# Kernel optimization log

Measured on AMD Instinct MI355X. Metric: run time of the kernel, lower is better.

Reference implementation:

```python
import jax, jax.numpy as jnp
import numpy as np

NUM_HEADS = 8
EPS = 1e-6


def setup_inputs() -> dict:
    key0 = jax.random.key(0)
    ks = jax.random.split(key0, 12)
    B, E, Hs, Ws, L = 8, 512, 32, 32, 1024
    s = 0.02
    return {
        "query": jax.random.normal(ks[0], (B, E, Hs, Ws), dtype=jnp.float32),
        "key": jax.random.normal(ks[1], (B, L, E), dtype=jnp.float32),
        "value": jax.random.normal(ks[2], (B, L, E), dtype=jnp.float32),
        # 1x1 conv for Q (kernel_size=1) stored as (E_out, E_in)
        "Wq": jax.random.normal(ks[3], (E, E), dtype=jnp.float32) * s,
        "bq": jnp.zeros((E,), dtype=jnp.float32),
        "Wk": jax.random.normal(ks[4], (E, E), dtype=jnp.float32) * s,
        "bk": jnp.zeros((E,), dtype=jnp.float32),
        "Wv": jax.random.normal(ks[5], (E, E), dtype=jnp.float32) * s,
        "bv": jnp.zeros((E,), dtype=jnp.float32),
        # out_conv: 1x1 conv + RMSNorm gain
        "Wo": jax.random.normal(ks[6], (E, E), dtype=jnp.float32) * s,
        "bo": jnp.zeros((E,), dtype=jnp.float32),
        "g": jnp.ones((E,), dtype=jnp.float32),
    }


def reference(query, key, value, Wq, bq, Wk, bk, Wv, bv, Wo, bo, g):
    B, E, Hs, Ws = query.shape
    H = NUM_HEADS
    Dh = E // H
    N = Hs * Ws
    # Q: 1x1 conv == per-pixel linear over channels
    Q = jnp.einsum('oi,bihw->bohw', Wq, query) + bq[None, :, None, None]
    # K, V: linear on last dim
    K = key @ Wk.T + bk      # (B, L, E)
    V = value @ Wv.T + bv    # (B, L, E)
    # faithful to torch .view: row-major reshape then transpose(2,3)
    Qh = Q.reshape(B, H, Dh, N).transpose(0, 1, 3, 2)        # (B, H, N, Dh)
    Kh = K.reshape(B, H, Dh, -1).transpose(0, 1, 3, 2)       # (B, H, L, Dh)
    Vh = V.reshape(B, H, Dh, -1).transpose(0, 1, 3, 2)       # (B, H, L, Dh)
    scores = jnp.einsum('bhnd,bhmd->bhnm', Qh, Kh) / jnp.sqrt(jnp.float32(Dh))
    attn = jax.nn.softmax(scores, axis=-1)
    out = jnp.einsum('bhnm,bhmd->bhnd', attn, Vh)            # (B, H, N, Dh)
    out = out.transpose(0, 1, 3, 2).reshape(B, E, Hs, Ws)
    # out_conv: 1x1 conv then channel-wise RMSNorm
    out = jnp.einsum('oi,bihw->bohw', Wo, out) + bo[None, :, None, None]
    rms = jnp.sqrt(jnp.mean(out * out, axis=1, keepdims=True) + EPS)
    return out / rms * g[None, :, None, None]
```

## Files before the change

kernel.cpp:

```cpp
#include <hip/hip_runtime.h>
#include <hip/hip_bf16.h>

namespace {

constexpr int kB  = 8;
constexpr int kE  = 512;
constexpr int kH  = 8;
constexpr int kDh = 64;
constexpr int kN  = 1024;
constexpr int kL  = 1024;

typedef __attribute__((ext_vector_type(8))) short short8;
typedef __attribute__((ext_vector_type(4))) float f32x4;
typedef __attribute__((ext_vector_type(4))) unsigned short ushort4v;

__device__ __forceinline__ unsigned short f2bf(float f) {
  unsigned u = __builtin_bit_cast(unsigned, f);
  u = (u + 0x7fffu + ((u >> 16) & 1u)) >> 16;
  return (unsigned short)u;
}

__device__ __forceinline__ f32x4 mfma16(short8 a, short8 b, f32x4 c) {
  return __builtin_amdgcn_mfma_f32_16x16x32_bf16(a, b, c, 0, 0, 0);
}

__device__ __forceinline__ void gl_lds16(const unsigned short* g, unsigned short* l) {
  __builtin_amdgcn_global_load_lds(
      (const __attribute__((address_space(1))) unsigned int*)g,
      (__attribute__((address_space(3))) unsigned int*)l, 16, 0, 0);
}

__global__ __launch_bounds__(256)
void convert_w(const float* __restrict__ w0, const float* __restrict__ w1,
               const float* __restrict__ w2, const float* __restrict__ w3,
               unsigned short* __restrict__ dst)
{
  const float* s = (blockIdx.y == 0) ? w0 : (blockIdx.y == 1) ? w1
                  : (blockIdx.y == 2) ? w2 : w3;
  unsigned short* d = dst + (size_t)blockIdx.y * 262144;
  const size_t i = ((size_t)blockIdx.x * 256 + threadIdx.x) * 4;
  const float4 v = *(const float4*)(s + i);
  ushort4v o = { f2bf(v.x), f2bf(v.y), f2bf(v.z), f2bf(v.w) };
  *(ushort4v*)(d + i) = o;
}

__global__ __launch_bounds__(256)
void convert_kv(const float* __restrict__ k, const float* __restrict__ v,
                unsigned short* __restrict__ dst)
{
  const float* s = blockIdx.y ? v : k;
  unsigned short* d = dst + (size_t)blockIdx.y * 4194304;
  const int flat = blockIdx.x * 256 + threadIdx.x;
  #pragma unroll
  for (int it = 0; it < 4; ++it) {
    const size_t i = ((size_t)flat + (size_t)it * 262144) * 4;
    const float4 x = *(const float4*)(s + i);
    ushort4v o = { f2bf(x.x), f2bf(x.y), f2bf(x.z), f2bf(x.w) };
    *(ushort4v*)(d + i) = o;
  }
}

__global__ __launch_bounds__(256)
void convert_qT(const float* __restrict__ q, unsigned short* __restrict__ qT)
{
  const int b = blockIdx.z, e0 = blockIdx.y * 32, n0 = blockIdx.x * 32;
  __shared__ float T[32][33];
  const int r  = threadIdx.x >> 3;
  const int c4 = (threadIdx.x & 7) * 4;
  const float4 v = *(const float4*)&q[((size_t)b * kE + e0 + r) * kN + n0 + c4];
  T[r][c4+0] = v.x; T[r][c4+1] = v.y; T[r][c4+2] = v.z; T[r][c4+3] = v.w;
  __syncthreads();
  ushort4v o = { f2bf(T[c4+0][r]), f2bf(T[c4+1][r]),
                 f2bf(T[c4+2][r]), f2bf(T[c4+3][r]) };
  *(ushort4v*)&qT[((size_t)b * kN + n0 + r) * kE + e0 + c4] = o;
}

__global__ __launch_bounds__(256)
void qkv_proj(const unsigned short* __restrict__ Wb4,
              const float* __restrict__ bq, const float* __restrict__ bk,
              const float* __restrict__ bv,
              const unsigned short* __restrict__ qT,
              const unsigned short* __restrict__ keyB,
              const unsigned short* __restrict__ valB,
              unsigned short* __restrict__ Qh,
              unsigned short* __restrict__ Kh,
              unsigned short* __restrict__ Vt)
{
  const int b    = blockIdx.z;
  const int mode = blockIdx.y >> 2;
  const int o0   = (blockIdx.y & 3) * 128;
  const int c0   = blockIdx.x * 128;
  const int wid  = threadIdx.x >> 6;
  const int lane = threadIdx.x & 63;
  const int lr = lane & 15, lg = lane >> 4;
  const int rbase = (wid >> 1) * 64;
  const int cbase = (wid & 1) * 64;

  __shared__ unsigned short smem[18432];

  const unsigned short* Wb   = Wb4 + (size_t)mode * 262144;
  const float*          bias = (mode == 0) ? bq : (mode == 1) ? bk : bv;
  const unsigned short* X    = (mode == 0) ? qT : (mode == 1) ? keyB : valB;

  const unsigned short* Wg = Wb + (size_t)o0 * kE;
  const unsigned short* Xg = X + ((size_t)b * 1024 + c0) * kE;

  const int srow = lane >> 2;
  const int sch  = lane & 3;

  auto stage = [&](int buf, int k0) {
    #pragma unroll
    for (int c = 0; c < 2; ++c) {
      const int row = wid * 32 + c * 16 + srow;
      const int koff = k0 + (((sch) ^ (row & 3)) << 3);
      gl_lds16(Wg + (size_t)row * kE + koff,
               &smem[buf * 8192 + (wid * 32 + c * 16) * 32]);
      gl_lds16(Xg + (size_t)row * kE + koff,
               &smem[buf * 8192 + 4096 + (wid * 32 + c * 16) * 32]);
    }
  };

  const f32x4 z = {0.f, 0.f, 0.f, 0.f};
  f32x4 acc[4][4];
  #pragma unroll
  for (int i = 0; i < 4; ++i)
    #pragma unroll
    for (int j = 0; j < 4; ++j) acc[i][j] = z;

  stage(0, 0);
  __syncthreads();

  for (int kt = 0; kt < 16; ++kt) {
    const int buf = kt & 1;
    if (kt < 15) stage(buf ^ 1, (kt + 1) * 32);

    short8 a[4], bfr[4];
    #pragma unroll
    for (int fr = 0; fr < 4; ++fr) {
      const int row = rbase + fr * 16 + lr;
      a[fr] = *(const short8*)&smem[buf * 8192 + row * 32 + ((lg ^ (row & 3)) << 3)];
    }
    #pragma unroll
    for (int fc = 0; fc < 4; ++fc) {
      const int row = cbase + fc * 16 + lr;
      bfr[fc] = *(const short8*)&smem[buf * 8192 + 4096 + row * 32 + ((lg ^ (row & 3)) << 3)];
    }
    #pragma unroll
    for (int fr = 0; fr < 4; ++fr)
      #pragma unroll
      for (int fc = 0; fc < 4; ++fc)
        acc[fr][fc] = mfma16(a[fr], bfr[fc], acc[fr][fc]);

    __syncthreads();
  }

  unsigned short* Ts = smem;
  #pragma unroll
  for (int fr = 0; fr < 4; ++fr) {
    #pragma unroll
    for (int j = 0; j < 4; ++j) {
      const int ol = rbase + fr * 16 + 4 * lg + j;
      const int o  = o0 + ol;
      const float bvv = bias[o];
      #pragma unroll
      for (int fc = 0; fc < 4; ++fc) {
        const int cl = cbase + fc * 16 + lr;
        float val = acc[fr][fc][j] + bvv;
        int addr;
        if (mode == 0) {
          const int hl = ol >> 6, d = o & 63;
          const int r = hl * 128 + cl;
          addr = r * 72 + ((((d >> 3) ^ (r & 7)) << 3) | (d & 7));
          val *= 0.125f;
        } else if (mode == 1) {
          const int seg = cl & 1, d = cl >> 1;
          const int r = seg * 128 + ol;
          addr = r * 72 + ((((d >> 3) ^ (r & 7)) << 3) | (d & 7));
        } else {
          const int r = cl;
          addr = r * 136 + ((((ol >> 3) ^ (r & 15)) << 3) | (ol & 7));
        }
        Ts[addr] = f2bf(val);
      }
    }
  }
  __syncthreads();

  const int hseg = c0 >> 7;
  #pragma unroll
  for (int it = 0; it < 8; ++it) {
    const int q = it * 256 + threadIdx.x;
    if (mode != 2) {
      const int r = q >> 3, ch = q & 7;
      const short8 vv = *(const short8*)&Ts[r * 72 + ((ch ^ (r & 7)) << 3)];
      if (mode == 0) {
        const int hl = r >> 7, n = r & 127;
        *(short8*)&Qh[((size_t)(b * kH + (o0 >> 6) + hl) * kN + c0 + n) * kDh + ch * 8] = vv;
      } else {
        const int seg = r >> 7, ml = r & 127;
        *(short8*)&Kh[((size_t)(b * kH + hseg) * kL + seg * 512 + o0 + ml) * kDh + ch * 8] = vv;
      }
    } else {
      const int r = q >> 4, ch = q & 15;
      const short8 vv = *(const short8*)&Ts[r * 136 + ((ch ^ (r & 15)) << 3)];
      const int d = r >> 1, half = r & 1;
      *(short8*)&Vt[((size_t)(b * kH + hseg) * kDh + d) * kL + half * 512 + o0 + ch * 8] = vv;
    }
  }
}

__global__ __launch_bounds__(256)
void attn_mfma(const unsigned short* __restrict__ Qh,
               const unsigned short* __restrict__ Kh,
               const unsigned short* __restrict__ Vt,
               unsigned short* __restrict__ AO)
{
  const int bh = blockIdx.x;
  const int h = bh & 7, b = bh >> 3;
  const int n0 = blockIdx.y * 128;
  const int tid  = threadIdx.x;
  const int wid  = tid >> 6;
  const int lane = tid & 63;
  const int lr = lane & 15, lg = lane >> 4;

  __shared__ unsigned short Ks[2][64 * 64];
  __shared__ unsigned short Vs[2][64 * 64];
  __shared__ unsigned short Pst[4][2][16 * 72];

  const unsigned short* Qp = Qh + ((size_t)(b * kH + h) * kN + n0 + wid * 32) * kDh;
  const unsigned short* Kp = Kh + (size_t)(b * kH + h) * kL * kDh;
  const unsigned short* Vp = Vt + (size_t)(b * kH + h) * kDh * kL;

  short8 aq[2][2];
  #pragma unroll
  for (int rf = 0; rf < 2; ++rf) {
    aq[rf][0] = *(const short8*)(Qp + (size_t)(rf * 16 + lr) * kDh + lg * 8);
    aq[rf][1] = *(const short8*)(Qp + (size_t)(rf * 16 + lr) * kDh + 32 + lg * 8);
  }

  const int srow8 = lane >> 3;
  const int sc16  = lane & 7;

  auto stageK = [&](int buf, int m0) {
    #pragma unroll
    for (int c = 0; c < 2; ++c) {
      const int row = wid * 16 + c * 8 + srow8;
      const unsigned short* src =
          Kp + (size_t)(m0 + row) * kDh + ((sc16 ^ (row & 7)) << 3);
      gl_lds16(src, &Ks[buf][(wid * 16 + c * 8) * 64]);
    }
  };
  auto stageV = [&](int buf, int m0) {
    #pragma unroll
    for (int c = 0; c < 2; ++c) {
      const int row = wid * 16 + c * 8 + srow8;
      const unsigned short* src =
          Vp + (size_t)row * kL + m0 + ((sc16 ^ (row & 7)) << 3);
      gl_lds16(src, &Vs[buf][(wid * 16 + c * 8) * 64]);
    }
  };

  const f32x4 z = {0.f, 0.f, 0.f, 0.f};
  f32x4 oacc[2][4];
  #pragma unroll
  for (int rf = 0; rf < 2; ++rf)
    #pragma unroll
    for (int dt = 0; dt < 4; ++dt) oacc[rf][dt] = z;
  f32x4 psum[2] = {z, z};

  stageK(0, 0);
  stageV(0, 0);
  __syncthreads();

  for (int kt = 0; kt < 16; ++kt) {
    const int cur = kt & 1;
    if (kt < 15) {
      stageK(cur ^ 1, (kt + 1) * 64);
      stageV(cur ^ 1, (kt + 1) * 64);
    }

    #pragma unroll
    for (int rf = 0; rf < 2; ++rf) {
      f32x4 s[4] = {z, z, z, z};
      #pragma unroll
      for (int t = 0; t < 4; ++t) {
        const int row = t * 16 + lr;
        const short8 bk0 = *(const short8*)&Ks[cur][row * 64 + (((lg    ) ^ (row & 7)) << 3)];
        const short8 bk1 = *(const short8*)&Ks[cur][row * 64 + (((4 + lg) ^ (row & 7)) << 3)];
        s[t] = mfma16(aq[rf][0], bk0, s[t]);
        s[t] = mfma16(aq[rf][1], bk1, s[t]);
      }
      #pragma unroll
      for (int t = 0; t < 4; ++t)
        #pragma unroll
        for (int j = 0; j < 4; ++j) {
          const float p = __expf(s[t][j]);
          psum[rf][j] += p;
          Pst[wid][rf][(4 * lg + j) * 72 + 16 * t + lr] = f2bf(p);
        }
    }

    #pragma unroll
    for (int rf = 0; rf < 2; ++rf) {
      const short8 ap0 = *(const short8*)&Pst[wid][rf][lr * 72 + lg * 8];
      const short8 ap1 = *(const short8*)&Pst[wid][rf][lr * 72 + 32 + lg * 8];
      #pragma unroll
      for (int dt = 0; dt < 4; ++dt) {
        const int row = dt * 16 + lr;
        const short8 bv0 = *(const short8*)&Vs[cur][row * 64 + (((lg    ) ^ (row & 7)) << 3)];
        const short8 bv1 = *(const short8*)&Vs[cur][row * 64 + (((4 + lg) ^ (row & 7)) << 3)];
        oacc[rf][dt] = mfma16(ap0, bv0, oacc[rf][dt]);
        oacc[rf][dt] = mfma16(ap1, bv1, oacc[rf][dt]);
      }
    }

    __syncthreads();
  }

  #pragma unroll
  for (int rf = 0; rf < 2; ++rf)
    #pragma unroll
    for (int j = 0; j < 4; ++j) {
      float ps = psum[rf][j];
      ps += __shfl_xor(ps, 1);
      ps += __shfl_xor(ps, 2);
      ps += __shfl_xor(ps, 4);
      ps += __shfl_xor(ps, 8);
      psum[rf][j] = 1.0f / ps;
    }
  #pragma unroll
  for (int rf = 0; rf < 2; ++rf)
    #pragma unroll
    for (int dt = 0; dt < 4; ++dt)
      #pragma unroll
      for (int j = 0; j < 4; ++j) {
        const int n = n0 + wid * 32 + rf * 16 + 4 * lg + j;
        AO[((size_t)(b * kN + n)) * kE + h * kDh + dt * 16 + lr] =
            f2bf(oacc[rf][dt][j] * psum[rf][j]);
      }
}

__global__ __launch_bounds__(512)
void oproj_rms(const unsigned short* __restrict__ Wob, const float* __restrict__ bo,
               const unsigned short* __restrict__ AO, const float* __restrict__ g,
               float* __restrict__ out)
{
  const int b  = blockIdx.y;
  const int c0 = blockIdx.x * 32;
  const int wid  = threadIdx.x >> 6;
  const int lane = threadIdx.x & 63;
  const int lr = lane & 15, lg = lane >> 4;

  const unsigned short* Wp = Wob + (size_t)(wid * 64 + lr) * kE;
  const unsigned short* Xp = AO + ((size_t)b * kN + c0 + lr) * kE;

  const f32x4 z = {0.f, 0.f, 0.f, 0.f};
  f32x4 acc[4][2];
  #pragma unroll
  for (int i = 0; i < 4; ++i) { acc[i][0] = z; acc[i][1] = z; }

  for (int k0 = 0; k0 < kE; k0 += 32) {
    short8 a[4], bfr[2];
    #pragma unroll
    for (int fr = 0; fr < 4; ++fr)
      a[fr] = *(const short8*)(Wp + (size_t)fr * 16 * kE + k0 + lg * 8);
    #pragma unroll
    for (int fc = 0; fc < 2; ++fc)
      bfr[fc] = *(const short8*)(Xp + (size_t)fc * 16 * kE + k0 + lg * 8);
    #pragma unroll
    for (int fr = 0; fr < 4; ++fr)
      #pragma unroll
      for (int fc = 0; fc < 2; ++fc)
        acc[fr][fc] = mfma16(a[fr], bfr[fc], acc[fr][fc]);
  }

  float ss[2] = {0.f, 0.f};
  #pragma unroll
  for (int fr = 0; fr < 4; ++fr) {
    #pragma unroll
    for (int j = 0; j < 4; ++j) {
      const int o = wid * 64 + fr * 16 + 4 * lg + j;
      const float bvv = bo[o];
      #pragma unroll
      for (int fc = 0; fc < 2; ++fc) {
        const float v = acc[fr][fc][j] + bvv;
        acc[fr][fc][j] = v;
        ss[fc] = fmaf(v, v, ss[fc]);
      }
    }
  }
  #pragma unroll
  for (int fc = 0; fc < 2; ++fc) {
    ss[fc] += __shfl_xor(ss[fc], 16);
    ss[fc] += __shfl_xor(ss[fc], 32);
  }

  __shared__ float ssb[8][32];
  if (lg == 0) {
    ssb[wid][0 * 16 + lr] = ss[0];
    ssb[wid][1 * 16 + lr] = ss[1];
  }
  __syncthreads();

  float rinv[2];
  #pragma unroll
  for (int fc = 0; fc < 2; ++fc) {
    float tot = 0.f;
    #pragma unroll
    for (int w = 0; w < 8; ++w) tot += ssb[w][fc * 16 + lr];
    rinv[fc] = 1.0f / sqrtf(tot * (1.0f / 512.0f) + 1e-6f);
  }

  #pragma unroll
  for (int fr = 0; fr < 4; ++fr)
    #pragma unroll
    for (int j = 0; j < 4; ++j) {
      const int o = wid * 64 + fr * 16 + 4 * lg + j;
      const float gv = g[o];
      #pragma unroll
      for (int fc = 0; fc < 2; ++fc) {
        const int c = c0 + fc * 16 + lr;
        out[((size_t)b * kE + o) * kN + c] = acc[fr][fc][j] * rinv[fc] * gv;
      }
    }
}

}

extern "C" void kernel_launch(void* const* d_in, const int* in_sizes, int n_in,
                              void* d_out, int out_size, void* d_ws, size_t ws_size,
                              hipStream_t stream)
{
  const float* query = (const float*)d_in[0];
  const float* key   = (const float*)d_in[1];
  const float* value = (const float*)d_in[2];
  const float* Wq    = (const float*)d_in[3];
  const float* bq    = (const float*)d_in[4];
  const float* Wk    = (const float*)d_in[5];
  const float* bk    = (const float*)d_in[6];
  const float* Wv    = (const float*)d_in[7];
  const float* bv    = (const float*)d_in[8];
  const float* Wo    = (const float*)d_in[9];
  const float* bo    = (const float*)d_in[10];
  const float* g     = (const float*)d_in[11];
  float* out = (float*)d_out;

  char* w = (char*)d_ws;
  unsigned short* qT   = (unsigned short*)(w);
  unsigned short* keyB = (unsigned short*)(w + ((size_t)8 << 20));
  unsigned short* valB = (unsigned short*)(w + ((size_t)16 << 20));
  unsigned short* Qh   = (unsigned short*)(w + ((size_t)24 << 20));
  unsigned short* Kh   = (unsigned short*)(w + ((size_t)32 << 20));
  unsigned short* Vt   = (unsigned short*)(w + ((size_t)40 << 20));
  unsigned short* Wb   = (unsigned short*)(w + ((size_t)48 << 20));
  unsigned short* AO   = qT;

  const dim3 blk(256);
  convert_w <<<dim3(256, 4),    blk, 0, stream>>>(Wq, Wk, Wv, Wo, Wb);
  convert_kv<<<dim3(1024, 2),   blk, 0, stream>>>(key, value, keyB);
  convert_qT<<<dim3(32, 16, 8), blk, 0, stream>>>(query, qT);

  qkv_proj  <<<dim3(8, 12, 8),  blk, 0, stream>>>(Wb, bq, bk, bv, qT, keyB, valB,
                                                  Qh, Kh, Vt);
  attn_mfma <<<dim3(64, 8),     blk, 0, stream>>>(Qh, Kh, Vt, AO);
  oproj_rms <<<dim3(32, 8),     dim3(512), 0, stream>>>(Wb + 786432, bo, AO, g, out);
}
```

Measured before the change: 199.7 us.

## Merge conversion kernels and stage out-projection through LDS with double buffering

Three separate fp32-to-bf16 conversion launches are merged into one flat-grid kernel, which cuts launch overhead and lets the pieces run concurrently. The out-projection+RMSNorm kernel is rewritten to use 256 threads and 16 columns per block, doubling the grid. It stages W and activation tiles into swizzled LDS with async global_load_lds double buffering instead of direct global vector loads. The risk is extra syncthreads per k-step and reduced per-block reuse of W across columns.

```diff
diff --git a/kernel.cpp b/kernel.cpp
--- a/kernel.cpp
+++ b/kernel.cpp
@@ -31,48 +31,49 @@
 }
 
 __global__ __launch_bounds__(256)
-void convert_w(const float* __restrict__ w0, const float* __restrict__ w1,
-               const float* __restrict__ w2, const float* __restrict__ w3,
-               unsigned short* __restrict__ dst)
+void convert_all(const float* __restrict__ q, const float* __restrict__ k,
+                 const float* __restrict__ v,
+                 const float* __restrict__ w0, const float* __restrict__ w1,
+                 const float* __restrict__ w2, const float* __restrict__ w3,
+                 unsigned short* __restrict__ qT,
+                 unsigned short* __restrict__ kvB,
+                 unsigned short* __restrict__ wB)
 {
-  const float* s = (blockIdx.y == 0) ? w0 : (blockIdx.y == 1) ? w1
-                  : (blockIdx.y == 2) ? w2 : w3;
-  unsigned short* d = dst + (size_t)blockIdx.y * 262144;
-  const size_t i = ((size_t)blockIdx.x * 256 + threadIdx.x) * 4;
-  const float4 v = *(const float4*)(s + i);
-  ushort4v o = { f2bf(v.x), f2bf(v.y), f2bf(v.z), f2bf(v.w) };
-  *(ushort4v*)(d + i) = o;
-}
-
-__global__ __launch_bounds__(256)
-void convert_kv(const float* __restrict__ k, const float* __restrict__ v,
-                unsigned short* __restrict__ dst)
-{
-  const float* s = blockIdx.y ? v : k;
-  unsigned short* d = dst + (size_t)blockIdx.y * 4194304;
-  const int flat = blockIdx.x * 256 + threadIdx.x;
-  #pragma unroll
-  for (int it = 0; it < 4; ++it) {
-    const size_t i = ((size_t)flat + (size_t)it * 262144) * 4;
-    const float4 x = *(const float4*)(s + i);
-    ushort4v o = { f2bf(x.x), f2bf(x.y), f2bf(x.z), f2bf(x.w) };
+  __shared__ float T[32][33];
+  const int id = blockIdx.x;
+  if (id < 4096) {
+    const int n0 = (id & 31) * 32, e0 = ((id >> 5) & 15) * 32, b = id >> 9;
+    const int r  = threadIdx.x >> 3;
+    const int c4 = (threadIdx.x & 7) * 4;
+    const float4 x = *(const float4*)&q[((size_t)b * kE + e0 + r) * kN + n0 + c4];
+    T[r][c4+0] = x.x; T[r][c4+1] = x.y; T[r][c4+2] = x.z; T[r][c4+3] = x.w;
+    __syncthreads();
+    ushort4v o = { f2bf(T[c4+0][r]), f2bf(T[c4+1][r]),
+                   f2bf(T[c4+2][r]), f2bf(T[c4+3][r]) };
+    *(ushort4v*)&qT[((size_t)b * kN + n0 + r) * kE + e0 + c4] = o;
+  } else if (id < 6144) {
+    const int kk = id - 4096;
+    const int x = kk & 1023, y = kk >> 10;
+    const float* s = y ? v : k;
+    unsigned short* d = kvB + (size_t)y * 4194304;
+    const int flat = x * 256 + threadIdx.x;
+    #pragma unroll
+    for (int it = 0; it < 4; ++it) {
+      const size_t i = ((size_t)flat + (size_t)it * 262144) * 4;
+      const float4 xv = *(const float4*)(s + i);
+      ushort4v o = { f2bf(xv.x), f2bf(xv.y), f2bf(xv.z), f2bf(xv.w) };
+      *(ushort4v*)(d + i) = o;
+    }
+  } else {
+    const int kk = id - 6144;
+    const int x = kk & 255, y = kk >> 8;
+    const float* s = (y == 0) ? w0 : (y == 1) ? w1 : (y == 2) ? w2 : w3;
+    unsigned short* d = wB + (size_t)y * 262144;
+    const size_t i = ((size_t)x * 256 + threadIdx.x) * 4;
+    const float4 xv = *(const float4*)(s + i);
+    ushort4v o = { f2bf(xv.x), f2bf(xv.y), f2bf(xv.z), f2bf(xv.w) };
     *(ushort4v*)(d + i) = o;
   }
-}
-
-__global__ __launch_bounds__(256)
-void convert_qT(const float* __restrict__ q, unsigned short* __restrict__ qT)
-{
-  const int b = blockIdx.z, e0 = blockIdx.y * 32, n0 = blockIdx.x * 32;
-  __shared__ float T[32][33];
-  const int r  = threadIdx.x >> 3;
-  const int c4 = (threadIdx.x & 7) * 4;
-  const float4 v = *(const float4*)&q[((size_t)b * kE + e0 + r) * kN + n0 + c4];
-  T[r][c4+0] = v.x; T[r][c4+1] = v.y; T[r][c4+2] = v.z; T[r][c4+3] = v.w;
-  __syncthreads();
-  ushort4v o = { f2bf(T[c4+0][r]), f2bf(T[c4+1][r]),
-                 f2bf(T[c4+2][r]), f2bf(T[c4+3][r]) };
-  *(ushort4v*)&qT[((size_t)b * kN + n0 + r) * kE + e0 + c4] = o;
 }
 
 __global__ __launch_bounds__(256)
@@ -340,89 +341,97 @@
       }
 }
 
-__global__ __launch_bounds__(512)
+__global__ __launch_bounds__(256)
 void oproj_rms(const unsigned short* __restrict__ Wob, const float* __restrict__ bo,
                const unsigned short* __restrict__ AO, const float* __restrict__ g,
                float* __restrict__ out)
 {
   const int b  = blockIdx.y;
-  const int c0 = blockIdx.x * 32;
+  const int c0 = blockIdx.x * 16;
   const int wid  = threadIdx.x >> 6;
   const int lane = threadIdx.x & 63;
   const int lr = lane & 15, lg = lane >> 4;
 
-  const unsigned short* Wp = Wob + (size_t)(wid * 64 + lr) * kE;
-  const unsigned short* Xp = AO + ((size_t)b * kN + c0 + lr) * kE;
+  __shared__ unsigned short As[2][256 * 32];
+  __shared__ unsigned short Bs[2][16 * 32];
+  __shared__ float ssb[4][16];
+
+  const int srow = lane >> 2;
+  const int sch  = lane & 3;
+
+  auto stage = [&](int buf, int pbase, int k0) {
+    #pragma unroll
+    for (int cc = 0; cc < 4; ++cc) {
+      const int r = wid * 64 + cc * 16 + srow;
+      const int koff = k0 + ((sch ^ (r & 3)) << 3);
+      gl_lds16(Wob + (size_t)(pbase + r) * kE + koff,
+               &As[buf][(wid * 64 + cc * 16) * 32]);
+    }
+    if (wid == 0) {
+      const int koff = k0 + ((sch ^ (srow & 3)) << 3);
+      gl_lds16(AO + ((size_t)b * kN + c0 + srow) * kE + koff, &Bs[buf][0]);
+    }
+  };
 
   const f32x4 z = {0.f, 0.f, 0.f, 0.f};
-  f32x4 acc[4][2];
-  #pragma unroll
-  for (int i = 0; i < 4; ++i) { acc[i][0] = z; acc[i][1] = z; }
-
-  for (int k0 = 0; k0 < kE; k0 += 32) {
-    short8 a[4], bfr[2];
+  f32x4 acc0[4] = {z, z, z, z};
+  f32x4 acc1[4] = {z, z, z, z};
+
+  stage(0, 0, 0);
+  __syncthreads();
+
+  #pragma unroll
+  for (int p = 0; p < 2; ++p) {
+    for (int kt = 0; kt < 16; ++kt) {
+      const int buf = (p * 16 + kt) & 1;
+      if (kt < 15)     stage(buf ^ 1, p * 256, (kt + 1) * 32);
+      else if (p == 0) stage(buf ^ 1, 256, 0);
+
+      short8 a[4];
+      #pragma unroll
+      for (int fr = 0; fr < 4; ++fr) {
+        const int r = wid * 64 + fr * 16 + lr;
+        a[fr] = *(const short8*)&As[buf][r * 32 + ((lg ^ (r & 3)) << 3)];
+      }
+      const short8 bf = *(const short8*)&Bs[buf][lr * 32 + ((lg ^ (lr & 3)) << 3)];
+      #pragma unroll
+      for (int fr = 0; fr < 4; ++fr) {
+        if (p == 0) acc0[fr] = mfma16(a[fr], bf, acc0[fr]);
+        else        acc1[fr] = mfma16(a[fr], bf, acc1[fr]);
+      }
+      __syncthreads();
+    }
+  }
+
+  float ss = 0.f;
+  #pragma unroll
+  for (int p = 0; p < 2; ++p)
     #pragma unroll
     for (int fr = 0; fr < 4; ++fr)
-      a[fr] = *(const short8*)(Wp + (size_t)fr * 16 * kE + k0 + lg * 8);
-    #pragma unroll
-    for (int fc = 0; fc < 2; ++fc)
-      bfr[fc] = *(const short8*)(Xp + (size_t)fc * 16 * kE + k0 + lg * 8);
+      #pragma unroll
+      for (int j = 0; j < 4; ++j) {
+        const int o = p * 256 + wid * 64 + fr * 16 + 4 * lg + j;
+        float v = (p == 0 ? acc0[fr][j] : acc1[fr][j]) + bo[o];
+        if (p == 0) acc0[fr][j] = v; else acc1[fr][j] = v;
+        ss = fmaf(v, v, ss);
+      }
+  ss += __shfl_xor(ss, 16);
+  ss += __shfl_xor(ss, 32);
+  if (lg == 0) ssb[wid][lr] = ss;
+  __syncthreads();
+  const float tot = ssb[0][lr] + ssb[1][lr] + ssb[2][lr] + ssb[3][lr];
+  const float rinv = 1.0f / sqrtf(tot * (1.0f / 512.0f) + 1e-6f);
+
+  #pragma unroll
+  for (int p = 0; p < 2; ++p)
     #pragma unroll
     for (int fr = 0; fr < 4; ++fr)
       #pragma unroll
-      for (int fc = 0; fc < 2; ++fc)
-        acc[fr][fc] = mfma16(a[fr], bfr[fc], acc[fr][fc]);
-  }
-
-  float ss[2] = {0.f, 0.f};
-  #pragma unroll
-  for (int fr = 0; fr < 4; ++fr) {
-    #pragma unroll
-    for (int j = 0; j < 4; ++j) {
-      const int o = wid * 64 + fr * 16 + 4 * lg + j;
-      const float bvv = bo[o];
-      #pragma unroll
-      for (int fc = 0; fc < 2; ++fc) {
-        const float v = acc[fr][fc][j] + bvv;
-        acc[fr][fc][j] = v;
-        ss[fc] = fmaf(v, v, ss[fc]);
-      }
-    }
-  }
-  #pragma unroll
-  for (int fc = 0; fc < 2; ++fc) {
-    ss[fc] += __shfl_xor(ss[fc], 16);
-    ss[fc] += __shfl_xor(ss[fc], 32);
-  }
-
-  __shared__ float ssb[8][32];
-  if (lg == 0) {
-    ssb[wid][0 * 16 + lr] = ss[0];
-    ssb[wid][1 * 16 + lr] = ss[1];
-  }
-  __syncthreads();
-
-  float rinv[2];
-  #pragma unroll
-  for (int fc = 0; fc < 2; ++fc) {
-    float tot = 0.f;
-    #pragma unroll
-    for (int w = 0; w < 8; ++w) tot += ssb[w][fc * 16 + lr];
-    rinv[fc] = 1.0f / sqrtf(tot * (1.0f / 512.0f) + 1e-6f);
-  }
-
-  #pragma unroll
-  for (int fr = 0; fr < 4; ++fr)
-    #pragma unroll
-    for (int j = 0; j < 4; ++j) {
-      const int o = wid * 64 + fr * 16 + 4 * lg + j;
-      const float gv = g[o];
-      #pragma unroll
-      for (int fc = 0; fc < 2; ++fc) {
-        const int c = c0 + fc * 16 + lr;
-        out[((size_t)b * kE + o) * kN + c] = acc[fr][fc][j] * rinv[fc] * gv;
-      }
-    }
+      for (int j = 0; j < 4; ++j) {
+        const int o = p * 256 + wid * 64 + fr * 16 + 4 * lg + j;
+        const float v = (p == 0 ? acc0[fr][j] : acc1[fr][j]);
+        out[((size_t)b * kE + o) * kN + c0 + lr] = v * rinv * g[o];
+      }
 }
 
 }
@@ -456,12 +465,10 @@
   unsigned short* AO   = qT;
 
   const dim3 blk(256);
-  convert_w <<<dim3(256, 4),    blk, 0, stream>>>(Wq, Wk, Wv, Wo, Wb);
-  convert_kv<<<dim3(1024, 2),   blk, 0, stream>>>(key, value, keyB);
-  convert_qT<<<dim3(32, 16, 8), blk, 0, stream>>>(query, qT);
-
-  qkv_proj  <<<dim3(8, 12, 8),  blk, 0, stream>>>(Wb, bq, bk, bv, qT, keyB, valB,
+  convert_all<<<dim3(7168),    blk, 0, stream>>>(query, key, value,
+                                                 Wq, Wk, Wv, Wo, qT, keyB, Wb);
+  qkv_proj   <<<dim3(8, 12, 8), blk, 0, stream>>>(Wb, bq, bk, bv, qT, keyB, valB,
                                                   Qh, Kh, Vt);
-  attn_mfma <<<dim3(64, 8),     blk, 0, stream>>>(Qh, Kh, Vt, AO);
-  oproj_rms <<<dim3(32, 8),     dim3(512), 0, stream>>>(Wb + 786432, bo, AO, g, out);
-}
+  attn_mfma  <<<dim3(64, 8),    blk, 0, stream>>>(Qh, Kh, Vt, AO);
+  oproj_rms  <<<dim3(64, 8),    blk, 0, stream>>>(Wb + 786432, bo, AO, g, out);
+}
```

Measured after the change: 188.5 us. 5.6% less time.
